# Optimization experiments

Hardware: AMD Instinct MI355X
Metric: run time of the kernel (lower is better)

Reference implementation:

```python
import jax, jax.numpy as jnp
import numpy as np

WS = 7  # window size
NH = 4  # num heads


def _relative_position_index(ws: int) -> np.ndarray:
    coords = np.stack(np.meshgrid(np.arange(ws), np.arange(ws), indexing='ij'))  # [2,ws,ws]
    coords = coords.reshape(2, -1)
    rel = coords[:, :, None] - coords[:, None, :]  # [2,N,N]
    rel = rel.transpose(1, 2, 0) + (ws - 1)
    rel[:, :, 0] *= 2 * ws - 1
    return rel.sum(-1)  # [N,N] in [0,(2ws-1)^2)


REL_IDX = _relative_position_index(WS)


def setup_inputs() -> dict:
    key = jax.random.key(0)
    k1, k2, k3, k4 = jax.random.split(key, 4)
    dim = 128
    x = jax.random.normal(k1, (64, 56, 56, dim), dtype=jnp.float32)
    qkv_w = jax.random.normal(k2, (dim, 3 * dim), dtype=jnp.float32) * (dim ** -0.5)
    qkv_b = jnp.zeros((3 * dim,), dtype=jnp.float32)
    proj_w = jax.random.normal(k3, (dim, dim), dtype=jnp.float32) * (dim ** -0.5)
    proj_b = jnp.zeros((dim,), dtype=jnp.float32)
    bias_table = jax.random.truncated_normal(k4, -2.0, 2.0, ((2 * WS - 1) ** 2, NH), dtype=jnp.float32) * 0.02
    return {"x": x, "qkv_w": qkv_w, "qkv_b": qkv_b, "proj_w": proj_w, "proj_b": proj_b, "bias_table": bias_table}


def reference(x, qkv_w, qkv_b, proj_w, proj_b, bias_table):
    B, H, W, C = x.shape
    ws, nh = WS, NH
    hd = C // nh
    N = ws * ws
    # window partition: [B*nWh*nWw, N, C]  (H,W divisible by ws -> no padding branch)
    xw = x.reshape(B, H // ws, ws, W // ws, ws, C).transpose(0, 1, 3, 2, 4, 5).reshape(-1, N, C)
    qkv = xw @ qkv_w + qkv_b  # [nW, N, 3C]
    qkv = qkv.reshape(-1, N, 3, nh, hd).transpose(2, 0, 3, 1, 4)  # [3, nW, nh, N, hd]
    q, k, v = qkv[0], qkv[1], qkv[2]
    attn = jnp.einsum('whqd,whkd->whqk', q, k) * (hd ** -0.5)  # [nW, nh, N, N]
    rel_bias = bias_table[REL_IDX.reshape(-1)].reshape(N, N, nh).transpose(2, 0, 1)  # [nh,N,N]
    attn = jax.nn.softmax(attn + rel_bias[None], axis=-1)
    out = jnp.einsum('whqk,whkd->whqd', attn, v)  # [nW, nh, N, hd]
    out = out.transpose(0, 2, 1, 3).reshape(-1, N, C)
    out = out @ proj_w + proj_b
    # window reverse
    out = out.reshape(B, H // ws, W // ws, ws, ws, C).transpose(0, 1, 3, 2, 4, 5).reshape(B, H, W, C)
    return out
```

## Files before the change

kernel.cpp:

```cpp
#include <hip/hip_runtime.h>
#include <hip/hip_bf16.h>

#define NTOK 49
#define NPAD 64
#define CDIM 128
#define C3   384
#define NHEAD 4
#define HDIM 32
#define SCALE 0.17677669529663687f

#define QS 136
#define VS 72
#define PS 72

typedef __attribute__((ext_vector_type(8))) __bf16 bf16x8;
typedef __attribute__((ext_vector_type(4))) __bf16 bf16x4;
typedef __attribute__((ext_vector_type(4))) float f32x4;

#define PIN(v) asm volatile("" : "+v"(v))


__global__ __launch_bounds__(256) void prep_kernel(
    const float* __restrict__ qkv_w, const float* __restrict__ proj_w,
    const float* __restrict__ bias_table,
    __bf16* __restrict__ qkvT, __bf16* __restrict__ projT, float* __restrict__ blut)
{
  int o = blockIdx.x * 256 + threadIdx.x;
  if (o < CDIM * C3) {
    int k = o / C3, n = o - k * C3;
    float v = qkv_w[o];
    if (n < CDIM) v *= SCALE;
    qkvT[n * CDIM + k] = (__bf16)v;
  } else if (o < CDIM * C3 + CDIM * CDIM) {
    int o2 = o - CDIM * C3;
    int k = o2 >> 7, n = o2 & 127;
    projT[n * CDIM + k] = (__bf16)proj_w[o2];
  } else if (o < CDIM * C3 + CDIM * CDIM + NHEAD * NPAD * NPAD) {
    int t3 = o - (CDIM * C3 + CDIM * CDIM);
    int hh = t3 >> 12, r = (t3 >> 6) & 63, c = t3 & 63;
    float v;
    if (c >= NTOK) v = -1e30f;
    else if (r >= NTOK) v = 0.0f;
    else {
      int idx = (r / 7 - c / 7 + 6) * 13 + (r % 7 - c % 7 + 6);
      v = bias_table[idx * NHEAD + hh];
    }
    blut[t3] = v;
  }
}

__global__ __launch_bounds__(512, 6) void attn_kernel(
    const float* __restrict__ x, const float* __restrict__ qkv_b,
    const float* __restrict__ proj_b,
    const __bf16* __restrict__ qkvT, const __bf16* __restrict__ projT,
    const float* __restrict__ blut, float* __restrict__ out)
{
  __shared__ __align__(16) char smem[53248];
  __bf16* qs_ = (__bf16*)smem;
  __bf16* ks_ = qs_ + NPAD * QS;
  __bf16* vT_ = ks_ + NPAD * QS;
  __bf16* xa_ = qs_;
  __bf16* Pm_ = vT_;
  __bf16* O_  = qs_;

  const int tid  = threadIdx.x;
  const int wave = tid >> 6;
  const int lane = tid & 63;
  const int l15  = lane & 15;
  const int lg   = lane >> 4;

  const int win = blockIdx.x;
  const int b  = win >> 6;
  const int wh = (win >> 3) & 7;
  const int ww = win & 7;
  const float* xbase = x + (((b * 56) + wh * 7) * 56 + ww * 7) * CDIM;

  #pragma unroll
  for (int p = 0; p < 2; ++p) {
    int L = p * 512 + tid;
    int r = L >> 4, c = L & 15;
    bf16x8 v8;
    if (r < NTOK) {
      const float* g = xbase + ((r / 7) * 56 + (r % 7)) * CDIM + c * 8;
      f32x4 x0 = *(const f32x4*)g;
      f32x4 x1 = *(const f32x4*)(g + 4);
      v8[0] = (__bf16)x0[0]; v8[1] = (__bf16)x0[1]; v8[2] = (__bf16)x0[2]; v8[3] = (__bf16)x0[3];
      v8[4] = (__bf16)x1[0]; v8[5] = (__bf16)x1[1]; v8[6] = (__bf16)x1[2]; v8[7] = (__bf16)x1[3];
    } else {
      #pragma unroll
      for (int q2 = 0; q2 < 8; ++q2) v8[q2] = (__bf16)0.0f;
    }
    *(bf16x8*)(xa_ + r * QS + c * 8) = v8;
  }

  const int nch = wave * 16 + l15;
  bf16x8 bwk[4], bwv[4];
  #pragma unroll
  for (int kt = 0; kt < 4; ++kt) {
    bwk[kt] = *(const bf16x8*)(qkvT + (CDIM + nch) * CDIM + kt * 32 + lg * 8);     PIN(bwk[kt]);
    bwv[kt] = *(const bf16x8*)(qkvT + (2 * CDIM + nch) * CDIM + kt * 32 + lg * 8); PIN(bwv[kt]);
  }
  const float kb = qkv_b[CDIM + nch];
  const float vb = qkv_b[2 * CDIM + nch];

  __syncthreads();

  #pragma unroll 2
  for (int mt = 0; mt < 4; ++mt) {
    bf16x8 a[4];
    #pragma unroll
    for (int kt = 0; kt < 4; ++kt)
      a[kt] = *(const bf16x8*)(xa_ + (mt * 16 + l15) * QS + kt * 32 + lg * 8);
    f32x4 ck, cv;
    ck[0]=0.f; ck[1]=0.f; ck[2]=0.f; ck[3]=0.f;
    cv[0]=0.f; cv[1]=0.f; cv[2]=0.f; cv[3]=0.f;
    #pragma unroll
    for (int kt = 0; kt < 4; ++kt) {
      ck = __builtin_amdgcn_mfma_f32_16x16x32_bf16(a[kt], bwk[kt], ck, 0, 0, 0);
      cv = __builtin_amdgcn_mfma_f32_16x16x32_bf16(a[kt], bwv[kt], cv, 0, 0, 0);
    }
    const int r0 = mt * 16 + lg * 4;
    #pragma unroll
    for (int i = 0; i < 4; ++i)
      ks_[(r0 + i) * QS + nch] = (__bf16)(ck[i] + kb);
    bf16x4 vv;
    #pragma unroll
    for (int i = 0; i < 4; ++i) vv[i] = (__bf16)(cv[i] + vb);
    *(bf16x4*)(vT_ + nch * VS + r0) = vv;
  }

  bf16x8 bwq[4];
  #pragma unroll
  for (int kt = 0; kt < 4; ++kt) {
    bwq[kt] = *(const bf16x8*)(qkvT + nch * CDIM + kt * 32 + lg * 8); PIN(bwq[kt]);
  }
  const float qb = qkv_b[nch] * SCALE;
  f32x4 aq[4];
  #pragma unroll
  for (int mt = 0; mt < 4; ++mt) {
    bf16x8 a[4];
    #pragma unroll
    for (int kt = 0; kt < 4; ++kt)
      a[kt] = *(const bf16x8*)(xa_ + (mt * 16 + l15) * QS + kt * 32 + lg * 8);
    aq[mt][0]=0.f; aq[mt][1]=0.f; aq[mt][2]=0.f; aq[mt][3]=0.f;
    #pragma unroll
    for (int kt = 0; kt < 4; ++kt)
      aq[mt] = __builtin_amdgcn_mfma_f32_16x16x32_bf16(a[kt], bwq[kt], aq[mt], 0, 0, 0);
  }

  __syncthreads();

  const int h  = wave & 3;
  const int hc = h * HDIM;
  bf16x8 akf[4];
  #pragma unroll
  for (int nt = 0; nt < 4; ++nt)
    akf[nt] = *(const bf16x8*)(ks_ + (nt * 16 + l15) * QS + hc + lg * 8);
  bf16x8 bv[2][2];
  #pragma unroll
  for (int n16 = 0; n16 < 2; ++n16)
    #pragma unroll
    for (int kt = 0; kt < 2; ++kt)
      bv[n16][kt] = *(const bf16x8*)(vT_ + (hc + n16 * 16 + l15) * VS + kt * 32 + lg * 8);

  #pragma unroll
  for (int mt = 0; mt < 4; ++mt) {
    const int r0 = mt * 16 + lg * 4;
    #pragma unroll
    for (int i = 0; i < 4; ++i)
      qs_[(r0 + i) * QS + nch] = (__bf16)(aq[mt][i] + qb);
  }

  __syncthreads();

  const float* blh = blut + h * 4096;
  __bf16* Pw = Pm_ + wave * 16 * PS;

  #pragma unroll
  for (int mi = 0; mi < 2; ++mi) {
    const int m0 = ((wave >> 2) * 2 + mi) * 16;

    f32x4 bias[4];
    #pragma unroll
    for (int nt = 0; nt < 4; ++nt)
      bias[nt] = *(const f32x4*)(blh + (m0 + l15) * 64 + nt * 16 + lg * 4);

    bf16x8 qf = *(const bf16x8*)(qs_ + (m0 + l15) * QS + hc + lg * 8);
    f32x4 s[4];
    #pragma unroll
    for (int nt = 0; nt < 4; ++nt) {
      f32x4 z; z[0]=0.f; z[1]=0.f; z[2]=0.f; z[3]=0.f;
      s[nt] = __builtin_amdgcn_mfma_f32_16x16x32_bf16(akf[nt], qf, z, 0, 0, 0);
    }

    float es[4][4];
    float p0 = 0.f, p1 = 0.f;
    #pragma unroll
    for (int nt = 0; nt < 4; ++nt) {
      #pragma unroll
      for (int i = 0; i < 4; ++i) {
        float e = __expf(s[nt][i] + bias[nt][i]);
        es[nt][i] = e;
        if (nt & 1) p1 += e; else p0 += e;
      }
      bf16x4 pv;
      #pragma unroll
      for (int i = 0; i < 4; ++i) pv[i] = (__bf16)es[nt][i];
      *(bf16x4*)(Pw + l15 * PS + nt * 16 + lg * 4) = pv;
    }
    float psum = p0 + p1;
    psum += __shfl_xor(psum, 16);
    psum += __shfl_xor(psum, 32);
    const float inv = __builtin_amdgcn_rcpf(psum);

    f32x4 o0, o1;
    o0[0]=0.f;o0[1]=0.f;o0[2]=0.f;o0[3]=0.f; o1[0]=0.f;o1[1]=0.f;o1[2]=0.f;o1[3]=0.f;
    #pragma unroll
    for (int kt = 0; kt < 2; ++kt) {
      bf16x8 ap = *(const bf16x8*)(Pw + l15 * PS + kt * 32 + lg * 8);
      o0 = __builtin_amdgcn_mfma_f32_16x16x32_bf16(ap, bv[0][kt], o0, 0, 0, 0);
      o1 = __builtin_amdgcn_mfma_f32_16x16x32_bf16(ap, bv[1][kt], o1, 0, 0, 0);
    }
    float invr[4];
    #pragma unroll
    for (int i = 0; i < 4; ++i) invr[i] = __shfl(inv, lg * 4 + i);
    const int r0 = m0 + lg * 4;
    #pragma unroll
    for (int i = 0; i < 4; ++i) {
      O_[(r0 + i) * QS + hc +      l15] = (__bf16)(o0[i] * invr[i]);
      O_[(r0 + i) * QS + hc + 16 + l15] = (__bf16)(o1[i] * invr[i]);
    }
  }

  const int nb2 = wave * 16;
  bf16x8 bp[4];
  #pragma unroll
  for (int kt = 0; kt < 4; ++kt) {
    bp[kt] = *(const bf16x8*)(projT + (nb2 + l15) * CDIM + kt * 32 + lg * 8);
    PIN(bp[kt]);
  }
  const float pb = proj_b[nb2 + l15];

  __syncthreads();

  float* outw = out + (((b * 56) + wh * 7) * 56 + ww * 7) * CDIM;
  #pragma unroll
  for (int mt = 0; mt < 4; ++mt) {
    bf16x8 ao[4];
    #pragma unroll
    for (int kt = 0; kt < 4; ++kt)
      ao[kt] = *(const bf16x8*)(O_ + (mt * 16 + l15) * QS + kt * 32 + lg * 8);
    f32x4 c0;
    c0[0]=0.f;c0[1]=0.f;c0[2]=0.f;c0[3]=0.f;
    #pragma unroll
    for (int kt = 0; kt < 4; ++kt)
      c0 = __builtin_amdgcn_mfma_f32_16x16x32_bf16(ao[kt], bp[kt], c0, 0, 0, 0);
    #pragma unroll
    for (int i = 0; i < 4; ++i) {
      const int r = mt * 16 + lg * 4 + i;
      if (r < NTOK) {
        float* po = outw + ((r / 7) * 56 + (r % 7)) * CDIM + nb2;
        po[l15] = c0[i] + pb;
      }
    }
  }
}

extern "C" void kernel_launch(void* const* d_in, const int* in_sizes, int n_in,
                              void* d_out, int out_size, void* d_ws, size_t ws_size,
                              hipStream_t stream) {
  const float* x          = (const float*)d_in[0];
  const float* qkv_w      = (const float*)d_in[1];
  const float* qkv_b      = (const float*)d_in[2];
  const float* proj_w     = (const float*)d_in[3];
  const float* proj_b     = (const float*)d_in[4];
  const float* bias_table = (const float*)d_in[5];

  __bf16* qkvT  = (__bf16*)d_ws;
  __bf16* projT = qkvT + C3 * CDIM;
  float*  blut  = (float*)((char*)d_ws + 131072);
  float*  out   = (float*)d_out;

  hipLaunchKernelGGL(prep_kernel, dim3(320), dim3(256), 0, stream,
                     qkv_w, proj_w, bias_table, qkvT, projT, blut);
  hipLaunchKernelGGL(attn_kernel, dim3(4096), dim3(512), 0, stream,
                     x, qkv_b, proj_b, qkvT, projT, blut, out);
}
```

Before: 262.1 us.

## Shrink LDS footprint with swizzled unpadded layout and register-resident Q/P

Reworks the fused window-attention kernel's shared memory from padded 64-row buffers to 49-row XOR-swizzled buffers, cutting LDS from 53KB to 38KB. Occupancy is raised to 8 blocks per CU. Q is kept in registers and moved between lanes with shuffles instead of going through LDS. The softmax probabilities are also fed straight from registers into the PV MFMA using a K=16 zero-padded trick instead of an LDS round trip. Softmax switches to exp2 with log2e folded into the Q weights and the bias table. These changes reduce LDS traffic and bank conflicts, at the cost of wasted MFMA work in PV and extra shuffles and register pressure.

```diff
diff --git a/kernel.cpp b/kernel.cpp
--- a/kernel.cpp
+++ b/kernel.cpp
@@ -2,22 +2,41 @@
 #include <hip/hip_bf16.h>
 
 #define NTOK 49
-#define NPAD 64
 #define CDIM 128
 #define C3   384
 #define NHEAD 4
 #define HDIM 32
 #define SCALE 0.17677669529663687f
-
-#define QS 136
-#define VS 72
-#define PS 72
+#define LOG2E 1.4426950408889634f
+#define SC2   (0.17677669529663687f * 1.4426950408889634f)
+#define TSV 52
 
 typedef __attribute__((ext_vector_type(8))) __bf16 bf16x8;
 typedef __attribute__((ext_vector_type(4))) __bf16 bf16x4;
 typedef __attribute__((ext_vector_type(4))) float f32x4;
 
 #define PIN(v) asm volatile("" : "+v"(v))
+
+__device__ __forceinline__ int swz(int b) { return b ^ ((b >> 4) & 0x70); }
+
+__device__ __forceinline__ f32x4 mfma32(bf16x8 a, bf16x8 b, f32x4 c) {
+  return __builtin_amdgcn_mfma_f32_16x16x32_bf16(a, b, c, 0, 0, 0);
+}
+__device__ __forceinline__ bf16x8 dup8(bf16x4 t) {
+  uint2 w = __builtin_bit_cast(uint2, t);
+  uint4 r; r.x = w.x; r.y = w.y; r.z = w.x; r.w = w.y;
+  return __builtin_bit_cast(bf16x8, r);
+}
+__device__ __forceinline__ bf16x8 zpad8(bf16x4 t) {
+  uint2 w = __builtin_bit_cast(uint2, t);
+  uint4 r; r.x = w.x; r.y = w.y; r.z = 0u; r.w = 0u;
+  return __builtin_bit_cast(bf16x8, r);
+}
+__device__ __forceinline__ unsigned pkbf(float lo, float hi) {
+  unsigned short a = __builtin_bit_cast(unsigned short, (__bf16)lo);
+  unsigned short b = __builtin_bit_cast(unsigned short, (__bf16)hi);
+  return ((unsigned)b << 16) | (unsigned)a;
+}
 
 
 __global__ __launch_bounds__(256) void prep_kernel(
@@ -29,13 +48,13 @@
   if (o < CDIM * C3) {
     int k = o / C3, n = o - k * C3;
     float v = qkv_w[o];
-    if (n < CDIM) v *= SCALE;
+    if (n < CDIM) v *= SC2;
     qkvT[n * CDIM + k] = (__bf16)v;
   } else if (o < CDIM * C3 + CDIM * CDIM) {
     int o2 = o - CDIM * C3;
     int k = o2 >> 7, n = o2 & 127;
     projT[n * CDIM + k] = (__bf16)proj_w[o2];
-  } else if (o < CDIM * C3 + CDIM * CDIM + NHEAD * NPAD * NPAD) {
+  } else if (o < CDIM * C3 + CDIM * CDIM + NHEAD * 64 * 64) {
     int t3 = o - (CDIM * C3 + CDIM * CDIM);
     int hh = t3 >> 12, r = (t3 >> 6) & 63, c = t3 & 63;
     float v;
@@ -45,29 +64,32 @@
       int idx = (r / 7 - c / 7 + 6) * 13 + (r % 7 - c % 7 + 6);
       v = bias_table[idx * NHEAD + hh];
     }
-    blut[t3] = v;
-  }
-}
-
-__global__ __launch_bounds__(512, 6) void attn_kernel(
+    blut[t3] = v * LOG2E;
+  }
+}
+
+__global__ __launch_bounds__(512, 8) void attn_kernel(
     const float* __restrict__ x, const float* __restrict__ qkv_b,
-    const float* __restrict__ proj_b,
-    const __bf16* __restrict__ qkvT, const __bf16* __restrict__ projT,
-    const float* __restrict__ blut, float* __restrict__ out)
+    const float* __restrict__ proj_b, const char* __restrict__ ws,
+    float* __restrict__ out)
 {
-  __shared__ __align__(16) char smem[53248];
-  __bf16* qs_ = (__bf16*)smem;
-  __bf16* ks_ = qs_ + NPAD * QS;
-  __bf16* vT_ = ks_ + NPAD * QS;
-  __bf16* xa_ = qs_;
-  __bf16* Pm_ = vT_;
-  __bf16* O_  = qs_;
+  __shared__ __align__(16) char smem[38400];
+  char*   xo_ = smem;
+  char*   ks_ = smem + 12544;
+  __bf16* vT_ = (__bf16*)(smem + 25088);
+
+  const __bf16* qkvT  = (const __bf16*)ws;
+  const __bf16* projT = (const __bf16*)(ws + 98304);
+  const float*  blut  = (const float*)(ws + 131072);
 
   const int tid  = threadIdx.x;
   const int wave = tid >> 6;
   const int lane = tid & 63;
   const int l15  = lane & 15;
   const int lg   = lane >> 4;
+  const int h    = wave & 3, half = wave >> 2;
+  const int hc   = h * HDIM;
+  const int chw  = wave * 16;
 
   const int win = blockIdx.x;
   const int b  = win >> 6;
@@ -75,191 +97,192 @@
   const int ww = win & 7;
   const float* xbase = x + (((b * 56) + wh * 7) * 56 + ww * 7) * CDIM;
 
-  #pragma unroll
-  for (int p = 0; p < 2; ++p) {
-    int L = p * 512 + tid;
-    int r = L >> 4, c = L & 15;
-    bf16x8 v8;
-    if (r < NTOK) {
-      const float* g = xbase + ((r / 7) * 56 + (r % 7)) * CDIM + c * 8;
-      f32x4 x0 = *(const f32x4*)g;
-      f32x4 x1 = *(const f32x4*)(g + 4);
-      v8[0] = (__bf16)x0[0]; v8[1] = (__bf16)x0[1]; v8[2] = (__bf16)x0[2]; v8[3] = (__bf16)x0[3];
-      v8[4] = (__bf16)x1[0]; v8[5] = (__bf16)x1[1]; v8[6] = (__bf16)x1[2]; v8[7] = (__bf16)x1[3];
-    } else {
-      #pragma unroll
-      for (int q2 = 0; q2 < 8; ++q2) v8[q2] = (__bf16)0.0f;
-    }
-    *(bf16x8*)(xa_ + r * QS + c * 8) = v8;
-  }
-
-  const int nch = wave * 16 + l15;
-  bf16x8 bwk[4], bwv[4];
+  {
+    int L = tid;
+    #pragma unroll
+    for (int p = 0; p < 2; ++p) {
+      if (L < 784) {
+        int r = L >> 4, c = L & 15;
+        const float* g = xbase + ((r / 7) * 56 + (r % 7)) * CDIM + c * 8;
+        f32x4 x0 = *(const f32x4*)g;
+        f32x4 x1 = *(const f32x4*)(g + 4);
+        bf16x8 v8;
+        v8[0] = (__bf16)x0[0]; v8[1] = (__bf16)x0[1]; v8[2] = (__bf16)x0[2]; v8[3] = (__bf16)x0[3];
+        v8[4] = (__bf16)x1[0]; v8[5] = (__bf16)x1[1]; v8[6] = (__bf16)x1[2]; v8[7] = (__bf16)x1[3];
+        *(bf16x8*)(xo_ + swz(r * 256 + c * 16)) = v8;
+      }
+      L += 512;
+    }
+  }
+
+  bf16x8 awk[4], awv[4];
   #pragma unroll
   for (int kt = 0; kt < 4; ++kt) {
-    bwk[kt] = *(const bf16x8*)(qkvT + (CDIM + nch) * CDIM + kt * 32 + lg * 8);     PIN(bwk[kt]);
-    bwv[kt] = *(const bf16x8*)(qkvT + (2 * CDIM + nch) * CDIM + kt * 32 + lg * 8); PIN(bwv[kt]);
-  }
-  const float kb = qkv_b[CDIM + nch];
-  const float vb = qkv_b[2 * CDIM + nch];
+    awk[kt] = *(const bf16x8*)(qkvT + (CDIM + chw + l15) * CDIM + kt * 32 + lg * 8);     PIN(awk[kt]);
+    awv[kt] = *(const bf16x8*)(qkvT + (2 * CDIM + chw + l15) * CDIM + kt * 32 + lg * 8); PIN(awv[kt]);
+  }
+  f32x4 kbv = *(const f32x4*)(qkv_b + CDIM + chw + lg * 4);
+  f32x4 vbv = *(const f32x4*)(qkv_b + 2 * CDIM + chw + lg * 4);
 
   __syncthreads();
 
-  #pragma unroll 2
+  #pragma unroll
   for (int mt = 0; mt < 4; ++mt) {
+    int tok = mt * 16 + l15;
+    int r = tok > 48 ? 48 : tok;
     bf16x8 a[4];
     #pragma unroll
     for (int kt = 0; kt < 4; ++kt)
-      a[kt] = *(const bf16x8*)(xa_ + (mt * 16 + l15) * QS + kt * 32 + lg * 8);
-    f32x4 ck, cv;
-    ck[0]=0.f; ck[1]=0.f; ck[2]=0.f; ck[3]=0.f;
-    cv[0]=0.f; cv[1]=0.f; cv[2]=0.f; cv[3]=0.f;
-    #pragma unroll
-    for (int kt = 0; kt < 4; ++kt) {
-      ck = __builtin_amdgcn_mfma_f32_16x16x32_bf16(a[kt], bwk[kt], ck, 0, 0, 0);
-      cv = __builtin_amdgcn_mfma_f32_16x16x32_bf16(a[kt], bwv[kt], cv, 0, 0, 0);
-    }
-    const int r0 = mt * 16 + lg * 4;
-    #pragma unroll
-    for (int i = 0; i < 4; ++i)
-      ks_[(r0 + i) * QS + nch] = (__bf16)(ck[i] + kb);
-    bf16x4 vv;
-    #pragma unroll
-    for (int i = 0; i < 4; ++i) vv[i] = (__bf16)(cv[i] + vb);
-    *(bf16x4*)(vT_ + nch * VS + r0) = vv;
-  }
-
-  bf16x8 bwq[4];
-  #pragma unroll
-  for (int kt = 0; kt < 4; ++kt) {
-    bwq[kt] = *(const bf16x8*)(qkvT + nch * CDIM + kt * 32 + lg * 8); PIN(bwq[kt]);
-  }
-  const float qb = qkv_b[nch] * SCALE;
-  f32x4 aq[4];
+      a[kt] = *(const bf16x8*)(xo_ + swz(r * 256 + kt * 64 + lg * 16));
+    f32x4 ck; ck[0]=0.f; ck[1]=0.f; ck[2]=0.f; ck[3]=0.f;
+    #pragma unroll
+    for (int kt = 0; kt < 4; ++kt) ck = mfma32(awk[kt], a[kt], ck);
+    if (tok <= 48) {
+      bf16x4 k4;
+      #pragma unroll
+      for (int i = 0; i < 4; ++i) k4[i] = (__bf16)(ck[i] + kbv[i]);
+      *(bf16x4*)(ks_ + swz(tok * 256 + (chw + lg * 4) * 2)) = k4;
+    }
+  }
+
   #pragma unroll
   for (int mt = 0; mt < 4; ++mt) {
+    int tok = mt * 16 + l15;
+    int r = tok > 48 ? 48 : tok;
     bf16x8 a[4];
     #pragma unroll
     for (int kt = 0; kt < 4; ++kt)
-      a[kt] = *(const bf16x8*)(xa_ + (mt * 16 + l15) * QS + kt * 32 + lg * 8);
-    aq[mt][0]=0.f; aq[mt][1]=0.f; aq[mt][2]=0.f; aq[mt][3]=0.f;
+      a[kt] = *(const bf16x8*)(xo_ + swz(r * 256 + kt * 64 + lg * 16));
+    f32x4 cv; cv[0]=0.f; cv[1]=0.f; cv[2]=0.f; cv[3]=0.f;
+    #pragma unroll
+    for (int kt = 0; kt < 4; ++kt) cv = mfma32(awv[kt], a[kt], cv);
+    if (tok <= 48) {
+      #pragma unroll
+      for (int i = 0; i < 4; ++i)
+        vT_[(chw + lg * 4 + i) * TSV + tok] = (__bf16)(cv[i] + vbv[i]);
+    } else if (tok <= 51) {
+      #pragma unroll
+      for (int i = 0; i < 4; ++i)
+        vT_[(chw + lg * 4 + i) * TSV + tok] = (__bf16)0.0f;
+    }
+  }
+
+  unsigned pkq[2][2][2];
+  #pragma unroll
+  for (int ct = 0; ct < 2; ++ct) {
+    bf16x8 awq[4];
     #pragma unroll
     for (int kt = 0; kt < 4; ++kt)
-      aq[mt] = __builtin_amdgcn_mfma_f32_16x16x32_bf16(a[kt], bwq[kt], aq[mt], 0, 0, 0);
+      awq[kt] = *(const bf16x8*)(qkvT + (hc + ct * 16 + l15) * CDIM + kt * 32 + lg * 8);
+    f32x4 qbv = *(const f32x4*)(qkv_b + hc + ct * 16 + lg * 4);
+    #pragma unroll
+    for (int mi = 0; mi < 2; ++mi) {
+      int tok = (2 * half + mi) * 16 + l15;
+      int r = tok > 48 ? 48 : tok;
+      bf16x8 a[4];
+      #pragma unroll
+      for (int kt = 0; kt < 4; ++kt)
+        a[kt] = *(const bf16x8*)(xo_ + swz(r * 256 + kt * 64 + lg * 16));
+      f32x4 qc; qc[0]=0.f; qc[1]=0.f; qc[2]=0.f; qc[3]=0.f;
+      #pragma unroll
+      for (int kt = 0; kt < 4; ++kt) qc = mfma32(awq[kt], a[kt], qc);
+      pkq[mi][ct][0] = pkbf(qc[0] + qbv[0] * SC2, qc[1] + qbv[1] * SC2);
+      pkq[mi][ct][1] = pkbf(qc[2] + qbv[2] * SC2, qc[3] + qbv[3] * SC2);
+    }
   }
 
   __syncthreads();
 
-  const int h  = wave & 3;
-  const int hc = h * HDIM;
+  const float* blh = blut + h * 4096;
   bf16x8 akf[4];
   #pragma unroll
-  for (int nt = 0; nt < 4; ++nt)
-    akf[nt] = *(const bf16x8*)(ks_ + (nt * 16 + l15) * QS + hc + lg * 8);
-  bf16x8 bv[2][2];
-  #pragma unroll
-  for (int n16 = 0; n16 < 2; ++n16)
-    #pragma unroll
-    for (int kt = 0; kt < 2; ++kt)
-      bv[n16][kt] = *(const bf16x8*)(vT_ + (hc + n16 * 16 + l15) * VS + kt * 32 + lg * 8);
-
-  #pragma unroll
-  for (int mt = 0; mt < 4; ++mt) {
-    const int r0 = mt * 16 + lg * 4;
-    #pragma unroll
-    for (int i = 0; i < 4; ++i)
-      qs_[(r0 + i) * QS + nch] = (__bf16)(aq[mt][i] + qb);
-  }
-
-  __syncthreads();
-
-  const float* blh = blut + h * 4096;
-  __bf16* Pw = Pm_ + wave * 16 * PS;
+  for (int nt = 0; nt < 4; ++nt) {
+    int rr = nt * 16 + l15; if (rr > 48) rr = 48;
+    akf[nt] = *(const bf16x8*)(ks_ + swz(rr * 256 + (hc + lg * 8) * 2));
+  }
 
   #pragma unroll
   for (int mi = 0; mi < 2; ++mi) {
-    const int m0 = ((wave >> 2) * 2 + mi) * 16;
-
-    f32x4 bias[4];
-    #pragma unroll
-    for (int nt = 0; nt < 4; ++nt)
-      bias[nt] = *(const f32x4*)(blh + (m0 + l15) * 64 + nt * 16 + lg * 4);
-
-    bf16x8 qf = *(const bf16x8*)(qs_ + (m0 + l15) * QS + hc + lg * 8);
-    f32x4 s[4];
+    const int m0 = (2 * half + mi) * 16;
+
+    unsigned bqw[4];
+    #pragma unroll
+    for (int d = 0; d < 4; ++d) {
+      int srcl = ((lg & 1) * 2 + (d >> 1)) * 16 + l15;
+      unsigned w0 = __shfl(pkq[mi][0][d & 1], srcl);
+      unsigned w1 = __shfl(pkq[mi][1][d & 1], srcl);
+      bqw[d] = (lane >= 32) ? w1 : w0;
+    }
+    uint4 bqv; bqv.x = bqw[0]; bqv.y = bqw[1]; bqv.z = bqw[2]; bqv.w = bqw[3];
+    bf16x8 bq8 = __builtin_bit_cast(bf16x8, bqv);
+
+    float psum = 0.f;
+    bf16x4 pa4[4];
     #pragma unroll
     for (int nt = 0; nt < 4; ++nt) {
+      f32x4 bias = *(const f32x4*)(blh + (m0 + l15) * 64 + nt * 16 + lg * 4);
       f32x4 z; z[0]=0.f; z[1]=0.f; z[2]=0.f; z[3]=0.f;
-      s[nt] = __builtin_amdgcn_mfma_f32_16x16x32_bf16(akf[nt], qf, z, 0, 0, 0);
-    }
-
-    float es[4][4];
-    float p0 = 0.f, p1 = 0.f;
-    #pragma unroll
-    for (int nt = 0; nt < 4; ++nt) {
-      #pragma unroll
-      for (int i = 0; i < 4; ++i) {
-        float e = __expf(s[nt][i] + bias[nt][i]);
-        es[nt][i] = e;
-        if (nt & 1) p1 += e; else p0 += e;
-      }
-      bf16x4 pv;
-      #pragma unroll
-      for (int i = 0; i < 4; ++i) pv[i] = (__bf16)es[nt][i];
-      *(bf16x4*)(Pw + l15 * PS + nt * 16 + lg * 4) = pv;
-    }
-    float psum = p0 + p1;
+      f32x4 s = mfma32(akf[nt], bq8, z);
+      float e0 = exp2f(s[0] + bias[0]);
+      float e1 = exp2f(s[1] + bias[1]);
+      float e2 = exp2f(s[2] + bias[2]);
+      float e3 = exp2f(s[3] + bias[3]);
+      psum += (e0 + e1) + (e2 + e3);
+      uint2 pw; pw.x = pkbf(e0, e1); pw.y = pkbf(e2, e3);
+      pa4[nt] = __builtin_bit_cast(bf16x4, pw);
+    }
     psum += __shfl_xor(psum, 16);
     psum += __shfl_xor(psum, 32);
     const float inv = __builtin_amdgcn_rcpf(psum);
 
-    f32x4 o0, o1;
-    o0[0]=0.f;o0[1]=0.f;o0[2]=0.f;o0[3]=0.f; o1[0]=0.f;o1[1]=0.f;o1[2]=0.f;o1[3]=0.f;
-    #pragma unroll
-    for (int kt = 0; kt < 2; ++kt) {
-      bf16x8 ap = *(const bf16x8*)(Pw + l15 * PS + kt * 32 + lg * 8);
-      o0 = __builtin_amdgcn_mfma_f32_16x16x32_bf16(ap, bv[0][kt], o0, 0, 0, 0);
-      o1 = __builtin_amdgcn_mfma_f32_16x16x32_bf16(ap, bv[1][kt], o1, 0, 0, 0);
-    }
-    float invr[4];
-    #pragma unroll
-    for (int i = 0; i < 4; ++i) invr[i] = __shfl(inv, lg * 4 + i);
-    const int r0 = m0 + lg * 4;
-    #pragma unroll
-    for (int i = 0; i < 4; ++i) {
-      O_[(r0 + i) * QS + hc +      l15] = (__bf16)(o0[i] * invr[i]);
-      O_[(r0 + i) * QS + hc + 16 + l15] = (__bf16)(o1[i] * invr[i]);
-    }
-  }
-
-  const int nb2 = wave * 16;
+    f32x4 ot0, ot1;
+    ot0[0]=0.f; ot0[1]=0.f; ot0[2]=0.f; ot0[3]=0.f;
+    ot1[0]=0.f; ot1[1]=0.f; ot1[2]=0.f; ot1[3]=0.f;
+    #pragma unroll
+    for (int nt = 0; nt < 4; ++nt) {
+      int tb = nt * 16 + lg * 4; if (tb > 48) tb = 48;
+      bf16x8 pb8 = zpad8(pa4[nt]);
+      bf16x4 v0 = *(const bf16x4*)(vT_ + (hc + l15) * TSV + tb);
+      bf16x4 v1 = *(const bf16x4*)(vT_ + (hc + 16 + l15) * TSV + tb);
+      ot0 = mfma32(dup8(v0), pb8, ot0);
+      ot1 = mfma32(dup8(v1), pb8, ot1);
+    }
+    const int rq = m0 + l15;
+    if (rq <= 48) {
+      #pragma unroll
+      for (int i = 0; i < 4; ++i) {
+        *(__bf16*)(xo_ + swz(rq * 256 + (hc + lg * 4 + i) * 2))      = (__bf16)(ot0[i] * inv);
+        *(__bf16*)(xo_ + swz(rq * 256 + (hc + 16 + lg * 4 + i) * 2)) = (__bf16)(ot1[i] * inv);
+      }
+    }
+  }
+
   bf16x8 bp[4];
   #pragma unroll
   for (int kt = 0; kt < 4; ++kt) {
-    bp[kt] = *(const bf16x8*)(projT + (nb2 + l15) * CDIM + kt * 32 + lg * 8);
+    bp[kt] = *(const bf16x8*)(projT + (chw + l15) * CDIM + kt * 32 + lg * 8);
     PIN(bp[kt]);
   }
-  const float pb = proj_b[nb2 + l15];
+  const float pb = proj_b[chw + l15];
 
   __syncthreads();
 
   float* outw = out + (((b * 56) + wh * 7) * 56 + ww * 7) * CDIM;
   #pragma unroll
   for (int mt = 0; mt < 4; ++mt) {
+    int rr = mt * 16 + l15; int rc = rr > 48 ? 48 : rr;
     bf16x8 ao[4];
     #pragma unroll
     for (int kt = 0; kt < 4; ++kt)
-      ao[kt] = *(const bf16x8*)(O_ + (mt * 16 + l15) * QS + kt * 32 + lg * 8);
-    f32x4 c0;
-    c0[0]=0.f;c0[1]=0.f;c0[2]=0.f;c0[3]=0.f;
-    #pragma unroll
-    for (int kt = 0; kt < 4; ++kt)
-      c0 = __builtin_amdgcn_mfma_f32_16x16x32_bf16(ao[kt], bp[kt], c0, 0, 0, 0);
+      ao[kt] = *(const bf16x8*)(xo_ + swz(rc * 256 + kt * 64 + lg * 16));
+    f32x4 c0; c0[0]=0.f; c0[1]=0.f; c0[2]=0.f; c0[3]=0.f;
+    #pragma unroll
+    for (int kt = 0; kt < 4; ++kt) c0 = mfma32(ao[kt], bp[kt], c0);
     #pragma unroll
     for (int i = 0; i < 4; ++i) {
       const int r = mt * 16 + lg * 4 + i;
       if (r < NTOK) {
-        float* po = outw + ((r / 7) * 56 + (r % 7)) * CDIM + nb2;
+        float* po = outw + ((r / 7) * 56 + (r % 7)) * CDIM + chw;
         po[l15] = c0[i] + pb;
       }
     }
@@ -284,5 +307,5 @@
   hipLaunchKernelGGL(prep_kernel, dim3(320), dim3(256), 0, stream,
                      qkv_w, proj_w, bias_table, qkvT, projT, blut);
   hipLaunchKernelGGL(attn_kernel, dim3(4096), dim3(512), 0, stream,
-                     x, qkv_b, proj_b, qkvT, projT, blut, out);
-}
+                     x, qkv_b, proj_b, (const char*)d_ws, out);
+}
```

Result: slower. 497.9 us (+90.0%).
